# Kernel optimization log

Hardware: AMD Instinct MI355X
Metric: run time of the kernel (lower is better)

The kernel has to match this reference:

```python
import jax, jax.numpy as jnp
import numpy as np

B, N, C, H = 4, 1024, 768, 12
D = C // H
SCALE = D ** -0.5


def setup_inputs() -> dict:
    key = jax.random.key(0)
    k1, k2, k3, k4 = jax.random.split(key, 4)
    x1 = jax.random.normal(k1, (B, N, C), dtype=jnp.float32)
    x2 = jax.random.normal(k2, (B, N, C), dtype=jnp.float32)
    # shared (dual-stream) Linear2 weights, torch nn.Linear layout: [out, in]
    W_qkv = jax.random.normal(k3, (3 * C, C), dtype=jnp.float32) * (C ** -0.5)
    b_qkv = jnp.zeros((3 * C,), dtype=jnp.float32)
    W_proj = jax.random.normal(k4, (C, C), dtype=jnp.float32) * (C ** -0.5)
    b_proj = jnp.zeros((C,), dtype=jnp.float32)
    return {"x1": x1, "x2": x2, "W_qkv": W_qkv, "b_qkv": b_qkv,
            "W_proj": W_proj, "b_proj": b_proj}


def _split_qkv(x, W_qkv, b_qkv):
    qkv = (x @ W_qkv.T + b_qkv).reshape(B, N, 3, H, D)
    qkv = jnp.transpose(qkv, (2, 0, 3, 1, 4))  # [3,B,H,N,D]
    return qkv[0], qkv[1], qkv[2]


def reference(x1, x2, W_qkv, b_qkv, W_proj, b_proj):
    q1, k1, v1 = _split_qkv(x1, W_qkv, b_qkv)
    q2, k2, v2 = _split_qkv(x2, W_qkv, b_qkv)
    # two score maps, combined before a single shared softmax
    s1 = jnp.einsum("bhqd,bhkd->bhqk", q1 * SCALE, k1)
    s2 = jnp.einsum("bhqd,bhkd->bhqk", q2 * SCALE, k2)
    attn = jax.nn.softmax(s1 + s2, axis=-1)  # [B,H,N,N]
    # same attention matrix applied to both value streams
    o1 = jnp.einsum("bhqk,bhkd->bhqd", attn, v1)
    o2 = jnpum = jnp.einsum("bhqk,bhkd->bhqd", attn, v2) if False else jnp.einsum("bhqk,bhkd->bhqd", attn, v2)
    o1 = jnp.transpose(o1, (0, 2, 1, 3)).reshape(B, N, C)
    o2 = jnp.transpose(o2, (0, 2, 1, 3)).reshape(B, N, C)
    y1 = o1 @ W_proj.T + b_proj
    y2 = o2 @ W_proj.T + b_proj
    return y1, y2
```

## Files before the change

### kernel.cpp

```cpp
#include <hip/hip_runtime.h>
#include <hip/hip_bf16.h>


typedef __bf16 bf16x8 __attribute__((ext_vector_type(8)));
typedef __bf16 bf16x4 __attribute__((ext_vector_type(4)));
typedef float  f32x4  __attribute__((ext_vector_type(4)));

__device__ __forceinline__ bf16x8 cvt8(const float* p) {
    f32x4 f0 = *(const f32x4*)p;
    f32x4 f1 = *(const f32x4*)(p + 4);
    bf16x8 r;
    r[0] = (__bf16)f0[0]; r[1] = (__bf16)f0[1]; r[2] = (__bf16)f0[2]; r[3] = (__bf16)f0[3];
    r[4] = (__bf16)f1[0]; r[5] = (__bf16)f1[1]; r[6] = (__bf16)f1[2]; r[7] = (__bf16)f1[3];
    return r;
}

__device__ __forceinline__ void async16(const __bf16* g, __bf16* l) {
    __builtin_amdgcn_global_load_lds(
        (const __attribute__((address_space(1))) void*)g,
        (__attribute__((address_space(3))) void*)l, 16, 0, 0);
}

__global__ __launch_bounds__(256)
void cvt3_k(const float* __restrict__ x1, const float* __restrict__ x2,
            const float* __restrict__ wq, __bf16* __restrict__ xc,
            __bf16* __restrict__ wqc)
{
    int bid = blockIdx.x;
    const float* src; __bf16* dst; int i;
    if (bid < 1536)      { src = x1; dst = xc;             i = (bid * 256 + threadIdx.x) * 8; }
    else if (bid < 3072) { src = x2; dst = xc + 3145728;   i = ((bid - 1536) * 256 + threadIdx.x) * 8; }
    else                 { src = wq; dst = wqc;            i = ((bid - 3072) * 256 + threadIdx.x) * 8; }
    *(bf16x8*)(dst + i) = cvt8(src + i);
}

__global__ __launch_bounds__(256)
void cvt_k(const float* __restrict__ src, __bf16* __restrict__ dst, int n) {
    int i = (blockIdx.x * 256 + threadIdx.x) * 8;
    if (i < n) *(bf16x8*)(dst + i) = cvt8(src + i);
}

__global__ __launch_bounds__(256)
void gemm_qkv_s(const __bf16* __restrict__ A, const __bf16* __restrict__ Wq,
                const float* __restrict__ bias,
                __bf16* __restrict__ qo, __bf16* __restrict__ ko,
                __bf16* __restrict__ vo, int st)
{
    constexpr int K = 768;
    __shared__ __bf16 As[128 * 32];
    __shared__ __bf16 Bs[128 * 32];

    const int t = threadIdx.x, w = t >> 6, lane = t & 63;
    const int l15 = lane & 15, quad = lane >> 4;
    const int wm = w >> 1, wn = w & 1;
    const int gx = blockIdx.x, gy = blockIdx.y;
    const int lrow = lane >> 2, lcol = (lane & 3) * 8;

    const __bf16* Ab = A  + (size_t)(gy * 128) * K;
    const __bf16* Bb = Wq + (size_t)(gx * 128) * K;

    f32x4 acc[4][4];
#pragma unroll
    for (int mi = 0; mi < 4; mi++)
#pragma unroll
        for (int ni = 0; ni < 4; ni++) acc[mi][ni] = f32x4{0.f, 0.f, 0.f, 0.f};

    for (int k0 = 0; k0 < K; k0 += 32) {
#pragma unroll
        for (int i = 0; i < 2; i++) {
            int r = w * 32 + i * 16 + lrow;
            async16(Ab + (size_t)r * K + k0 + lcol, &As[r * 32 + lcol]);
            async16(Bb + (size_t)r * K + k0 + lcol, &Bs[r * 32 + lcol]);
        }
        __syncthreads();
        bf16x8 af[4], bfr[4];
#pragma unroll
        for (int mi = 0; mi < 4; mi++)
            af[mi] = *(const bf16x8*)&As[(wm * 64 + mi * 16 + l15) * 32 + quad * 8];
#pragma unroll
        for (int ni = 0; ni < 4; ni++)
            bfr[ni] = *(const bf16x8*)&Bs[(wn * 64 + ni * 16 + l15) * 32 + quad * 8];
#pragma unroll
        for (int mi = 0; mi < 4; mi++)
#pragma unroll
            for (int ni = 0; ni < 4; ni++)
                acc[mi][ni] = __builtin_amdgcn_mfma_f32_16x16x32_bf16(af[mi], bfr[ni], acc[mi][ni], 0, 0, 0);
        __syncthreads();
    }

#pragma unroll
    for (int ni = 0; ni < 4; ni++) {
        int j     = gx * 128 + wn * 64 + ni * 16 + l15;
        int which = j / 768;
        int c     = j - which * 768;
        int h = c >> 6, d = c & 63;
        float bj  = bias[j];
#pragma unroll
        for (int mi = 0; mi < 4; mi++) {
#pragma unroll
            for (int r = 0; r < 4; r++) {
                int row = gy * 128 + wm * 64 + mi * 16 + quad * 4 + r;
                int b = row >> 10, tok = row & 1023;
                float val = acc[mi][ni][r] + bj;
                if (which == 0)
                    qo[((size_t)((st * 4 + b) * 12 + h) * 1024 + tok) * 64 + d] = (__bf16)(val * 0.125f);
                else if (which == 1)
                    ko[((size_t)((st * 4 + b) * 12 + h) * 1024 + tok) * 64 + d] = (__bf16)val;
                else
                    vo[((size_t)((st * 4 + b) * 12 + h) * 64 + d) * 1024 + tok] = (__bf16)val;
            }
        }
    }
}

__global__ __launch_bounds__(256)
void gemm_proj(const __bf16* __restrict__ A, const __bf16* __restrict__ Wp,
               const float* __restrict__ bias, float* __restrict__ out)
{
    constexpr int K = 768;
    __shared__ __bf16 As[128 * 32];
    __shared__ __bf16 Bs[128 * 32];

    const int t = threadIdx.x, w = t >> 6, lane = t & 63;
    const int l15 = lane & 15, quad = lane >> 4;
    const int wm = w >> 1, wn = w & 1;
    const int gx = blockIdx.x, gy = blockIdx.y;
    const int lrow = lane >> 2, lcol = (lane & 3) * 8;

    const __bf16* Ab = A  + (size_t)(gy * 128) * K;
    const __bf16* Bb = Wp + (size_t)(gx * 128) * K;

    f32x4 acc[4][4];
#pragma unroll
    for (int mi = 0; mi < 4; mi++)
#pragma unroll
        for (int ni = 0; ni < 4; ni++) acc[mi][ni] = f32x4{0.f, 0.f, 0.f, 0.f};

    for (int k0 = 0; k0 < K; k0 += 32) {
#pragma unroll
        for (int i = 0; i < 2; i++) {
            int r = w * 32 + i * 16 + lrow;
            async16(Ab + (size_t)r * K + k0 + lcol, &As[r * 32 + lcol]);
            async16(Bb + (size_t)r * K + k0 + lcol, &Bs[r * 32 + lcol]);
        }
        __syncthreads();
        bf16x8 af[4], bfr[4];
#pragma unroll
        for (int mi = 0; mi < 4; mi++)
            af[mi] = *(const bf16x8*)&As[(wm * 64 + mi * 16 + l15) * 32 + quad * 8];
#pragma unroll
        for (int ni = 0; ni < 4; ni++)
            bfr[ni] = *(const bf16x8*)&Bs[(wn * 64 + ni * 16 + l15) * 32 + quad * 8];
#pragma unroll
        for (int mi = 0; mi < 4; mi++)
#pragma unroll
            for (int ni = 0; ni < 4; ni++)
                acc[mi][ni] = __builtin_amdgcn_mfma_f32_16x16x32_bf16(af[mi], bfr[ni], acc[mi][ni], 0, 0, 0);
        __syncthreads();
    }

#pragma unroll
    for (int ni = 0; ni < 4; ni++) {
        int col  = gx * 128 + wn * 64 + ni * 16 + l15;
        float bj = bias[col];
#pragma unroll
        for (int mi = 0; mi < 4; mi++)
#pragma unroll
            for (int r = 0; r < 4; r++) {
                int row = gy * 128 + wm * 64 + mi * 16 + quad * 4 + r;
                out[(size_t)row * 768 + col] = acc[mi][ni][r] + bj;
            }
    }
}

__global__ __launch_bounds__(256)
void attn_k(const __bf16* __restrict__ qws, const __bf16* __restrict__ kws,
            const __bf16* __restrict__ vws, __bf16* __restrict__ ows)
{
    __shared__ __bf16 KVf[2][2][2][4][512];
    __shared__ __bf16 Ps[4][16 * 72];

    const int g  = blockIdx.x;
    const int qt = g / 48;
    const int bh = g % 48;
    const int b = bh / 12, h = bh % 12;
    const int t = threadIdx.x, w = t >> 6, lane = t & 63;
    const int l15 = lane & 15, quad = lane >> 4;

    const size_t head_off = (size_t)bh * 65536;
    const size_t ss       = (size_t)48 * 65536;

    bf16x8 qf[2][2];
#pragma unroll
    for (int s = 0; s < 2; s++)
#pragma unroll
        for (int kk = 0; kk < 2; kk++)
            qf[s][kk] = *(const bf16x8*)(qws + s * ss + head_off
                          + (size_t)(qt * 64 + w * 16 + l15) * 64 + kk * 32 + quad * 8);

    float lsum = 0.f;
    f32x4 accO[2][4];
#pragma unroll
    for (int s = 0; s < 2; s++)
#pragma unroll
        for (int mi = 0; mi < 4; mi++) accO[s][mi] = f32x4{0.f, 0.f, 0.f, 0.f};

    const __bf16* kbase = kws + head_off;
    const __bf16* vbase = vws + head_off;

    for (int kt = 0; kt < 16; kt++) {
        __syncthreads();
#pragma unroll
        for (int i = 0; i < 8; i++) {
            int f  = w * 8 + i;
            int kv = f >> 4, s = (f >> 3) & 1, kk = (f >> 2) & 1, mi = f & 3;
            const __bf16* gp;
            if (kv == 0)
                gp = kbase + s * ss + (size_t)(kt * 64 + mi * 16 + l15) * 64
                     + kk * 32 + quad * 8;
            else
                gp = vbase + s * ss + (size_t)(mi * 16 + l15) * 1024
                     + kt * 64 + kk * 32 + quad * 8;
            async16(gp, &KVf[kv][s][kk][mi][lane * 8]);
        }
        __syncthreads();

        f32x4 accS[4];
#pragma unroll
        for (int i = 0; i < 4; i++) accS[i] = f32x4{0.f, 0.f, 0.f, 0.f};
#pragma unroll
        for (int s = 0; s < 2; s++)
#pragma unroll
            for (int kk = 0; kk < 2; kk++) {
                bf16x8 kf[4];
#pragma unroll
                for (int mi = 0; mi < 4; mi++)
                    kf[mi] = *(const bf16x8*)&KVf[0][s][kk][mi][lane * 8];
#pragma unroll
                for (int mi = 0; mi < 4; mi++)
                    accS[mi] = __builtin_amdgcn_mfma_f32_16x16x32_bf16(kf[mi], qf[s][kk], accS[mi], 0, 0, 0);
            }

        float rs = 0.f;
        bf16x4 pk[4];
#pragma unroll
        for (int mi = 0; mi < 4; mi++)
#pragma unroll
            for (int r = 0; r < 4; r++) {
                float pv = __expf(accS[mi][r]);
                pk[mi][r] = (__bf16)pv;
                rs += pv;
            }
        lsum += rs;

#pragma unroll
        for (int mi = 0; mi < 4; mi++)
            *(bf16x4*)&Ps[w][l15 * 72 + mi * 16 + quad * 4] = pk[mi];

#pragma unroll
        for (int kk = 0; kk < 2; kk++) {
            bf16x8 pa = *(const bf16x8*)&Ps[w][l15 * 72 + kk * 32 + quad * 8];
#pragma unroll
            for (int s = 0; s < 2; s++)
#pragma unroll
                for (int mi = 0; mi < 4; mi++) {
                    bf16x8 vf = *(const bf16x8*)&KVf[1][s][kk][mi][lane * 8];
                    accO[s][mi] = __builtin_amdgcn_mfma_f32_16x16x32_bf16(vf, pa, accO[s][mi], 0, 0, 0);
                }
        }
    }

    lsum += __shfl_xor(lsum, 16);
    lsum += __shfl_xor(lsum, 32);
    float il = 1.f / lsum;

    const int tok = qt * 64 + w * 16 + l15;
#pragma unroll
    for (int s = 0; s < 2; s++)
#pragma unroll
        for (int mi = 0; mi < 4; mi++) {
            bf16x4 ov;
#pragma unroll
            for (int r = 0; r < 4; r++) ov[r] = (__bf16)(accO[s][mi][r] * il);
            *(bf16x4*)&ows[((size_t)((s * 4 + b) * 1024 + tok)) * 768
                           + h * 64 + mi * 16 + quad * 4] = ov;
        }
}

extern "C" void kernel_launch(void* const* d_in, const int* in_sizes, int n_in,
                              void* d_out, int out_size, void* d_ws, size_t ws_size,
                              hipStream_t stream)
{
    const float* x1    = (const float*)d_in[0];
    const float* x2    = (const float*)d_in[1];
    const float* Wqkv  = (const float*)d_in[2];
    const float* bqkv  = (const float*)d_in[3];
    const float* Wproj = (const float*)d_in[4];
    const float* bproj = (const float*)d_in[5];
    float* out = (float*)d_out;

    const size_t qkv_elems = (size_t)2 * 4 * 12 * 1024 * 64;
    __bf16* q_ws = (__bf16*)d_ws;
    __bf16* k_ws = q_ws + qkv_elems;
    __bf16* v_ws = k_ws + qkv_elems;
    __bf16* pool = v_ws + qkv_elems;
    __bf16* Wqc  = pool + 3145728;
    __bf16* o_ws = pool;
    __bf16* Wpc  = q_ws;
    __bf16* Xc   = (__bf16*)d_out;

    cvt3_k<<<3936, 256, 0, stream>>>(x1, x2, Wqkv, Xc, Wqc);
    gemm_qkv_s<<<dim3(18, 32), 256, 0, stream>>>(Xc, Wqc, bqkv, q_ws, k_ws, v_ws, 0);
    gemm_qkv_s<<<dim3(18, 32), 256, 0, stream>>>(Xc + 3145728, Wqc, bqkv, q_ws, k_ws, v_ws, 1);
    attn_k<<<768, 256, 0, stream>>>(q_ws, k_ws, v_ws, o_ws);
    cvt_k<<<288, 256, 0, stream>>>(Wproj, Wpc, 589824);
    gemm_proj<<<dim3(6, 64), 256, 0, stream>>>(o_ws, Wpc, bproj, out);
}
```

Before: 246.4 us.

## Merge QKV GEMM launches via grid z and process two key tiles per sync

The two per-stream QKV GEMM launches become one launch that uses blockIdx.z to select the stream, which removes a kernel launch and lets both streams' blocks fill the GPU together. The attention kernel now stages two 64-key K/V tiles per iteration, doubling the LDS buffer and halving the number of barrier pairs in the key loop. The cost is higher LDS usage per block, which may reduce occupancy, and more async loads issued per wave per iteration.

```diff
diff --git a/kernel.cpp b/kernel.cpp
--- a/kernel.cpp
+++ b/kernel.cpp
@@ -41,10 +41,10 @@
 }
 
 __global__ __launch_bounds__(256)
-void gemm_qkv_s(const __bf16* __restrict__ A, const __bf16* __restrict__ Wq,
+void gemm_qkv_s(const __bf16* __restrict__ Xc, const __bf16* __restrict__ Wq,
                 const float* __restrict__ bias,
                 __bf16* __restrict__ qo, __bf16* __restrict__ ko,
-                __bf16* __restrict__ vo, int st)
+                __bf16* __restrict__ vo)
 {
     constexpr int K = 768;
     __shared__ __bf16 As[128 * 32];
@@ -53,10 +53,10 @@
     const int t = threadIdx.x, w = t >> 6, lane = t & 63;
     const int l15 = lane & 15, quad = lane >> 4;
     const int wm = w >> 1, wn = w & 1;
-    const int gx = blockIdx.x, gy = blockIdx.y;
+    const int gx = blockIdx.x, gy = blockIdx.y, st = blockIdx.z;
     const int lrow = lane >> 2, lcol = (lane & 3) * 8;
 
-    const __bf16* Ab = A  + (size_t)(gy * 128) * K;
+    const __bf16* Ab = Xc + (size_t)st * 3145728 + (size_t)(gy * 128) * K;
     const __bf16* Bb = Wq + (size_t)(gx * 128) * K;
 
     f32x4 acc[4][4];
@@ -177,7 +177,7 @@
 void attn_k(const __bf16* __restrict__ qws, const __bf16* __restrict__ kws,
             const __bf16* __restrict__ vws, __bf16* __restrict__ ows)
 {
-    __shared__ __bf16 KVf[2][2][2][4][512];
+    __shared__ __bf16 KVf[2][2][2][2][4][512];
     __shared__ __bf16 Ps[4][16 * 72];
 
     const int g  = blockIdx.x;
@@ -208,65 +208,70 @@
     const __bf16* kbase = kws + head_off;
     const __bf16* vbase = vws + head_off;
 
-    for (int kt = 0; kt < 16; kt++) {
-        __syncthreads();
-#pragma unroll
-        for (int i = 0; i < 8; i++) {
-            int f  = w * 8 + i;
-            int kv = f >> 4, s = (f >> 3) & 1, kk = (f >> 2) & 1, mi = f & 3;
+    for (int kt2 = 0; kt2 < 8; kt2++) {
+        __syncthreads();
+#pragma unroll
+        for (int i = 0; i < 16; i++) {
+            int f    = w * 16 + i;
+            int tile = f >> 5, rem = f & 31;
+            int kv = rem >> 4, s = (rem >> 3) & 1, kk = (rem >> 2) & 1, mi = rem & 3;
+            int keyb = kt2 * 128 + tile * 64;
             const __bf16* gp;
             if (kv == 0)
-                gp = kbase + s * ss + (size_t)(kt * 64 + mi * 16 + l15) * 64
+                gp = kbase + s * ss + (size_t)(keyb + mi * 16 + l15) * 64
                      + kk * 32 + quad * 8;
             else
                 gp = vbase + s * ss + (size_t)(mi * 16 + l15) * 1024
-                     + kt * 64 + kk * 32 + quad * 8;
-            async16(gp, &KVf[kv][s][kk][mi][lane * 8]);
-        }
-        __syncthreads();
-
-        f32x4 accS[4];
-#pragma unroll
-        for (int i = 0; i < 4; i++) accS[i] = f32x4{0.f, 0.f, 0.f, 0.f};
-#pragma unroll
-        for (int s = 0; s < 2; s++)
+                     + keyb + kk * 32 + quad * 8;
+            async16(gp, &KVf[tile][kv][s][kk][mi][lane * 8]);
+        }
+        __syncthreads();
+
+#pragma unroll
+        for (int tile = 0; tile < 2; tile++) {
+            f32x4 accS[4];
+#pragma unroll
+            for (int i = 0; i < 4; i++) accS[i] = f32x4{0.f, 0.f, 0.f, 0.f};
+#pragma unroll
+            for (int s = 0; s < 2; s++)
+#pragma unroll
+                for (int kk = 0; kk < 2; kk++) {
+                    bf16x8 kf[4];
+#pragma unroll
+                    for (int mi = 0; mi < 4; mi++)
+                        kf[mi] = *(const bf16x8*)&KVf[tile][0][s][kk][mi][lane * 8];
+#pragma unroll
+                    for (int mi = 0; mi < 4; mi++)
+                        accS[mi] = __builtin_amdgcn_mfma_f32_16x16x32_bf16(kf[mi], qf[s][kk], accS[mi], 0, 0, 0);
+                }
+
+            float rs = 0.f;
+            bf16x4 pk[4];
+#pragma unroll
+            for (int mi = 0; mi < 4; mi++)
+#pragma unroll
+                for (int r = 0; r < 4; r++) {
+                    float pv = __expf(accS[mi][r]);
+                    pk[mi][r] = (__bf16)pv;
+                    rs += pv;
+                }
+            lsum += rs;
+
+#pragma unroll
+            for (int mi = 0; mi < 4; mi++)
+                *(bf16x4*)&Ps[w][l15 * 72 + mi * 16 + quad * 4] = pk[mi];
+
 #pragma unroll
             for (int kk = 0; kk < 2; kk++) {
-                bf16x8 kf[4];
-#pragma unroll
-                for (int mi = 0; mi < 4; mi++)
-                    kf[mi] = *(const bf16x8*)&KVf[0][s][kk][mi][lane * 8];
-#pragma unroll
-                for (int mi = 0; mi < 4; mi++)
-                    accS[mi] = __builtin_amdgcn_mfma_f32_16x16x32_bf16(kf[mi], qf[s][kk], accS[mi], 0, 0, 0);
+                bf16x8 pa = *(const bf16x8*)&Ps[w][l15 * 72 + kk * 32 + quad * 8];
+#pragma unroll
+                for (int s = 0; s < 2; s++)
+#pragma unroll
+                    for (int mi = 0; mi < 4; mi++) {
+                        bf16x8 vf = *(const bf16x8*)&KVf[tile][1][s][kk][mi][lane * 8];
+                        accO[s][mi] = __builtin_amdgcn_mfma_f32_16x16x32_bf16(vf, pa, accO[s][mi], 0, 0, 0);
+                    }
             }
-
-        float rs = 0.f;
-        bf16x4 pk[4];
-#pragma unroll
-        for (int mi = 0; mi < 4; mi++)
-#pragma unroll
-            for (int r = 0; r < 4; r++) {
-                float pv = __expf(accS[mi][r]);
-                pk[mi][r] = (__bf16)pv;
-                rs += pv;
-            }
-        lsum += rs;
-
-#pragma unroll
-        for (int mi = 0; mi < 4; mi++)
-            *(bf16x4*)&Ps[w][l15 * 72 + mi * 16 + quad * 4] = pk[mi];
-
-#pragma unroll
-        for (int kk = 0; kk < 2; kk++) {
-            bf16x8 pa = *(const bf16x8*)&Ps[w][l15 * 72 + kk * 32 + quad * 8];
-#pragma unroll
-            for (int s = 0; s < 2; s++)
-#pragma unroll
-                for (int mi = 0; mi < 4; mi++) {
-                    bf16x8 vf = *(const bf16x8*)&KVf[1][s][kk][mi][lane * 8];
-                    accO[s][mi] = __builtin_amdgcn_mfma_f32_16x16x32_bf16(vf, pa, accO[s][mi], 0, 0, 0);
-                }
         }
     }
 
@@ -310,8 +315,7 @@
     __bf16* Xc   = (__bf16*)d_out;
 
     cvt3_k<<<3936, 256, 0, stream>>>(x1, x2, Wqkv, Xc, Wqc);
-    gemm_qkv_s<<<dim3(18, 32), 256, 0, stream>>>(Xc, Wqc, bqkv, q_ws, k_ws, v_ws, 0);
-    gemm_qkv_s<<<dim3(18, 32), 256, 0, stream>>>(Xc + 3145728, Wqc, bqkv, q_ws, k_ws, v_ws, 1);
+    gemm_qkv_s<<<dim3(18, 32, 2), 256, 0, stream>>>(Xc, Wqc, bqkv, q_ws, k_ws, v_ws);
     attn_k<<<768, 256, 0, stream>>>(q_ws, k_ws, v_ws, o_ws);
     cvt_k<<<288, 256, 0, stream>>>(Wproj, Wpc, 589824);
     gemm_proj<<<dim3(6, 64), 256, 0, stream>>>(o_ws, Wpc, bproj, out);
```

Result: no change. 242.0 us (-1.8%).
